# Performance work log

Measured on AMD Instinct MI355X. Metric: run time of the kernel, lower is better.

Reference implementation:

```python
import math
import jax, jax.numpy as jnp
from jax import lax
import numpy as np

SIZE = 5      # kernel size == num_gaussian
MUL = 16      # multiplicity of 0e and 1o in irreps_in/out
IN_DIM = 4 * MUL  # 16 scalars + 16 vectors = 64


def real_sh(v, xp=jnp):
    """Real spherical harmonics l=0..3, component normalization (||Y_l||^2=2l+1
    on unit vectors), homogeneous polynomial form so the zero vector maps to
    (1,0,...,0). v: (...,3) -> (...,16)."""
    x = v[..., 0]; y = v[..., 1]; z = v[..., 2]
    r2 = x * x + y * y + z * z
    s3 = math.sqrt(3.0); s5 = math.sqrt(5.0); s15 = math.sqrt(15.0)
    s7 = math.sqrt(7.0); s105 = math.sqrt(105.0)
    c21 = 0.5 * math.sqrt(10.5)   # (1/2)sqrt(21/2)
    c35 = 0.5 * math.sqrt(17.5)   # (1/2)sqrt(35/2)
    out = [
        xp.ones_like(x),
        s3 * y, s3 * z, s3 * x,
        s15 * x * y, s15 * y * z, 0.5 * s5 * (3 * z * z - r2),
        s15 * x * z, 0.5 * s15 * (x * x - y * y),
        c35 * y * (3 * x * x - y * y), s105 * x * y * z,
        c21 * y * (5 * z * z - r2), 0.5 * s7 * z * (5 * z * z - 3 * r2),
        c21 * x * (5 * z * z - r2), 0.5 * s105 * z * (x * x - y * y),
        c35 * x * (x * x - 3 * y * y),
    ]
    return xp.stack(out, axis=-1)


def _wigner3j(l1, l2, l3, rng):
    """Unit-Frobenius-norm SO(3)-invariant 3-tensor in the real SH basis above,
    found as the nullspace of rotation-invariance constraints (fp64 numpy)."""
    dims = (2 * l1 + 1, 2 * l2 + 1, 2 * l3 + 1)
    n = dims[0] * dims[1] * dims[2]
    rows = []
    for _ in range(4):
        A = rng.standard_normal((3, 3))
        Q, _ = np.linalg.qr(A)
        if np.linalg.det(Q) < 0:
            Q = -Q
        X = rng.standard_normal((64, 3))
        X /= np.linalg.norm(X, axis=1, keepdims=True)
        YA = real_sh(X, np)
        YB = real_sh(X @ Q.T, np)
        Ds = []
        for l in (l1, l2, l3):
            sl = slice(l * l, (l + 1) * (l + 1))
            D = np.linalg.lstsq(YA[:, sl], YB[:, sl], rcond=None)[0].T
            Ds.append(D)
        rows.append(np.kron(Ds[0], np.kron(Ds[1], Ds[2])) - np.eye(n))
    _, _, Vt = np.linalg.svd(np.concatenate(rows, 0))
    w = Vt[-1]
    w = w * np.sign(w[np.argmax(np.abs(w))])  # deterministic sign
    w = w / np.linalg.norm(w)
    return w.reshape(dims).astype(np.float32)

_rng = np.random.default_rng(7)
W3J = {k: jnp.asarray(_wigner3j(*k, _rng))
       for k in [(0, 0, 0), (0, 1, 1), (1, 0, 1), (1, 1, 0), (1, 2, 1)]}


def setup_inputs() -> dict:
    key = jax.random.key(0)
    k1, k2, k3, k4 = jax.random.split(key, 4)
    return {
        "x": jax.random.normal(k1, (4, IN_DIM, 32, 32, 32), jnp.float32),
        "w_lin0": jax.random.normal(k2, (MUL, MUL), jnp.float32),
        "w_lin1": jax.random.normal(k3, (MUL, MUL), jnp.float32),
        "tp_weight": jax.random.normal(k4, (SIZE, 5 * MUL * MUL), jnp.float32),
    }


def reference(x, w_lin0, w_lin1, tp_weight):
    size, mul = SIZE, MUL
    # --- lattice buffers (d, sh) ---
    r = jnp.linspace(-1.0, 1.0, size)
    lat = jnp.stack(jnp.meshgrid(r, r, r, indexing="ij"), axis=-1)  # (s,s,s,3)
    d = jnp.sqrt(jnp.sum(lat * lat, axis=-1))
    v = lat / jnp.maximum(d, 1e-12)[..., None]
    sh = real_sh(v)  # (s,s,s,16)
    # --- gaussian radial basis -> per-voxel tp weights ---
    centers = jnp.linspace(0.0, 1.0, size)
    sigma = 1.0 / (size - 1)
    emb = jnp.exp(-jnp.square((d[..., None] - centers) / sigma)) / 1.12
    w = (emb @ tp_weight) * jnp.cos(jnp.pi * d)[..., None] / size ** 1.5
    W = w.reshape(size, size, size, 5, mul, mul)  # 5 tp instructions
    # path normalization: sqrt((2l_out+1)/fan_in), fan_in = sum mul1*mul2 per output
    f0 = math.sqrt(1.0 / (2 * mul))   # 0e output: 2 paths of fan 16
    f1 = math.sqrt(3.0 / (3 * mul))   # 1o output: 3 paths of fan 16

    def blk(C, ysl, Wp, f):
        # C: (2l1+1,2l2+1,2l3+1); ysl: (s,s,s,2l2+1); Wp: (s,s,s,mul,mul)
        t = f * jnp.einsum("abc,xyzb,xyzuw->xyzuawc", C, ysl, Wp)
        s = t.shape
        return t.reshape(size, size, size, s[3] * s[4], s[5] * s[6])

    y0 = sh[..., 0:1]; y1 = sh[..., 1:4]; y2 = sh[..., 4:9]
    b00 = blk(W3J[(0, 0, 0)], y0, W[..., 0, :, :], f0)   # 0e->0e (16,16)
    b01 = blk(W3J[(0, 1, 1)], y1, W[..., 1, :, :], f1)   # 0e->1o (16,48)
    b11a = blk(W3J[(1, 0, 1)], y0, W[..., 2, :, :], f1)  # 1o->1o (48,48)
    b10 = blk(W3J[(1, 1, 0)], y1, W[..., 3, :, :], f0)   # 1o->0e (48,16)
    b11b = blk(W3J[(1, 2, 1)], y2, W[..., 4, :, :], f1)  # 1o->1o (48,48)
    k = jnp.concatenate([
        jnp.concatenate([b00, b01], axis=-1),
        jnp.concatenate([b10, b11a + b11b], axis=-1)], axis=-2)  # (s,s,s,64,64)
    kernel = jnp.transpose(k, (4, 3, 0, 1, 2))  # oixyz
    # --- self-interaction (e3nn Linear, per-l block, 1/sqrt(fan_in)) ---
    B = x.shape[0]
    sp = x.shape[2:]
    inv = 1.0 / math.sqrt(mul)
    x0 = x[:, :mul]
    x1 = x[:, mul:].reshape(B, mul, 3, *sp)
    si0 = inv * jnp.einsum("uv,buxyz->bvxyz", w_lin0, x0)
    si1 = inv * jnp.einsum("uv,bumxyz->bvmxyz", w_lin1, x1)
    si = jnp.concatenate([si0, si1.reshape(B, 3 * mul, *sp)], axis=1)
    # --- conv3d (cross-correlation, padding size//2) ---
    conv = lax.conv_general_dilated(
        x, kernel, window_strides=(1, 1, 1),
        padding=[(size // 2, size // 2)] * 3,
        dimension_numbers=("NCDHW", "OIDHW", "NCDHW"))
    return si + 0.1 * conv
```

## Files before the change

kernel.cpp:

```cpp
#include <hip/hip_runtime.h>
#include <math.h>

typedef __attribute__((ext_vector_type(8))) short bf16x8;
typedef __attribute__((ext_vector_type(16))) float f32x16;
typedef __attribute__((ext_vector_type(4))) unsigned int u32x4;

#define XB 131072

__device__ __forceinline__ unsigned f2bf(float f) {
    union { float f; unsigned u; } v; v.f = f;
    return (v.u + 0x7FFFu + ((v.u >> 16) & 1u)) >> 16;
}

template<int VM6, int LG>
__device__ __forceinline__ void waitcnt_fence() {
    __builtin_amdgcn_s_waitcnt((VM6 & 15) | ((VM6 >> 4) << 14) | (7 << 4) | (LG << 8));
    __builtin_amdgcn_sched_barrier(0);
}

__global__ __launch_bounds__(256) void prep(
    const float* __restrict__ w_lin0,
    const float* __restrict__ w_lin1,
    const float* __restrict__ tp_weight,
    unsigned short* __restrict__ Kb3,
    const float* __restrict__ x,
    unsigned short* __restrict__ xbz)
{
    __shared__ float wsh[1280];
    __shared__ float y1s[3];
    __shared__ float Qs[9];
    __shared__ __align__(16) char xpose[32768];

    const int tid = (int)threadIdx.x;
    const int blk = (int)blockIdx.x;

    if (blk < 128) {
        const int tap = blk;
#define KIDX(o, i) ((((i) >> 3) * 128 + tap) * 512 + (o) * 8 + ((i) & 7))
        if (tap >= 125) {
            for (int n = tid; n < 4096; n += 256)
                Kb3[(n >> 9) * 65536 + tap * 512 + (n & 511)] = 0;
            return;
        }
        const int i1 = tap / 25, i2 = (tap / 5) % 5, i3 = tap % 5;
        const float X = -1.0f + 0.5f * (float)i1;
        const float Y = -1.0f + 0.5f * (float)i2;
        const float Z = -1.0f + 0.5f * (float)i3;
        const float d = sqrtf(X*X + Y*Y + Z*Z);
        const float dinv = 1.0f / fmaxf(d, 1e-12f);
        const float vx = X * dinv, vy = Y * dinv, vz = Z * dinv;
        const float r2 = vx*vx + vy*vy + vz*vz;

        if (tid == 0) {
            const float s3 = 1.7320508075688772f;
            const float s15 = 3.872983346207417f;
            y1s[0] = s3 * vy; y1s[1] = s3 * vz; y1s[2] = s3 * vx;
            float y2v0 = s15 * vx * vy;
            float y2v1 = s15 * vy * vz;
            float y2v2 = 1.118033988749895f * (3.0f * vz * vz - r2);
            float y2v3 = s15 * vx * vz;
            float y2v4 = 1.9364916731037085f * (vx * vx - vy * vy);
            const float INV10 = 0.31622776601683794f;
            const float INV30 = 0.18257418583505536f;
            Qs[0] = -y2v2 * INV30 - y2v4 * INV10;
            Qs[4] =  2.0f * y2v2 * INV30;
            Qs[8] = -y2v2 * INV30 + y2v4 * INV10;
            Qs[1] = Qs[3] = y2v1 * INV10;
            Qs[2] = Qs[6] = y2v0 * INV10;
            Qs[5] = Qs[7] = y2v3 * INV10;
        }

        float emb[5];
        #pragma unroll
        for (int e = 0; e < 5; ++e) {
            float t = (d - 0.25f * (float)e) * 4.0f;
            emb[e] = expf(-t * t) * (1.0f / 1.12f);
        }
        const float scale = cosf(3.14159265358979323846f * d) / 11.180339887498949f;

        for (int j = tid; j < 1280; j += 256) {
            float s = 0.0f;
            #pragma unroll
            for (int e = 0; e < 5; ++e) s += emb[e] * tp_weight[e * 1280 + j];
            wsh[j] = scale * s;
        }
        __syncthreads();

        const float F0   = 0.17677669529663687f;
        const float F1   = 0.25f;
        const float F0S3 = 0.10206207261596574f;
        const float F1S3 = 0.14433756729740646f;

        #pragma unroll 1
        for (int n = 0; n < 16; ++n) {
            int e = n * 256 + tid;
            int o = e & 63, i = e >> 6;
            float Kv;
            if (o < 16) {
                if (i < 16) {
                    Kv = F0 * wsh[0 * 256 + i * 16 + o];
                } else {
                    int u = (i - 16) / 3, a = (i - 16) % 3;
                    Kv = F0S3 * y1s[a] * wsh[3 * 256 + u * 16 + o];
                }
            } else {
                int wcol = (o - 16) / 3, c = (o - 16) % 3;
                if (i < 16) {
                    Kv = F1S3 * y1s[c] * wsh[1 * 256 + i * 16 + wcol];
                } else {
                    int u = (i - 16) / 3, a = (i - 16) % 3;
                    Kv = F1 * Qs[a * 3 + c] * wsh[4 * 256 + u * 16 + wcol];
                    if (a == c) Kv += F1S3 * wsh[2 * 256 + u * 16 + wcol];
                }
            }
            if (tap == 62) {
                if (o < 16) {
                    if (i < 16) Kv += 2.5f * w_lin0[i * 16 + o];
                } else if (i >= 16) {
                    int v = (o - 16) / 3, m = (o - 16) % 3;
                    int u = (i - 16) / 3, a = (i - 16) % 3;
                    if (a == m) Kv += 2.5f * w_lin1[u * 16 + v];
                }
            }
            Kb3[KIDX(o, i)] = (unsigned short)f2bf(Kv);
        }
#undef KIDX
        return;
    }

    const int blk2 = blk - 128;
    if (blk2 == 0 && tid < 64) xbz[tid] = 0;
    const int p = blk2 * 256 + tid;
    const int b = p >> 15, pos = p & 32767;
    const float* xp = x + ((size_t)b << 21) + pos;

    u32x4 dv[8];
    #pragma unroll
    for (int cg = 0; cg < 8; ++cg) {
        #pragma unroll
        for (int jj = 0; jj < 4; ++jj) {
            float f0 = xp[((size_t)(cg * 8 + 2 * jj)) << 15];
            float f1 = xp[((size_t)(cg * 8 + 2 * jj + 1)) << 15];
            dv[cg][jj] = f2bf(f0) | (f2bf(f1) << 16);
        }
    }
    #pragma unroll
    for (int cg = 0; cg < 8; ++cg)
        *(u32x4*)&xpose[tid * 128 + ((cg ^ (tid & 7)) << 4)] = dv[cg];
    __syncthreads();

    const int w = tid >> 6, l = tid & 63, q = l >> 3, cg = l & 7;
    #pragma unroll
    for (int it = 0; it < 8; ++it) {
        int tsrc = w * 64 + it * 8 + q;
        u32x4 c = *(const u32x4*)&xpose[tsrc * 128 + ((cg ^ (tsrc & 7)) << 4)];
        *(u32x4*)((char*)xbz + 128 + ((size_t)(blk2 * 256 + tsrc)) * 128 + cg * 16) = c;
    }
}

template<int P, int PLAST>
__device__ __forceinline__ void kstep2(
    const int (&nbase)[2], int abase, bool thv,
    bf16x8 (&Ar)[2][2], bf16x8 (&Br)[2][2], f32x16 (&acc)[2][2])
{
    if constexpr (P < PLAST) {
        constexpr int Q = P + 1;
        constexpr int t0 = 2 * Q;
        constexpr int t1 = (2 * Q + 1 == 125) ? 124 : 2 * Q + 1;
        constexpr int dA = ((t0 / 25) * 160 + ((t0 / 5) % 5) * 20 + (t0 % 5)) * 16;
        constexpr int dB = ((t1 / 25) * 160 + ((t1 / 5) % 5) * 20 + (t1 % 5)) * 16;
        #pragma unroll
        for (int mo = 0; mo < 2; ++mo) {
            int a = Q * 2048 + abase + mo * 512;
            asm volatile("ds_read_b128 %0, %1" : "=v"(Ar[Q & 1][mo]) : "v"(a));
        }
        int dsel = thv ? dB : dA;
        #pragma unroll
        for (int np = 0; np < 2; ++np) {
            int a = nbase[np] + dsel;
            asm volatile("ds_read_b128 %0, %1" : "=v"(Br[Q & 1][np]) : "v"(a));
        }
    }
    waitcnt_fence<63, (P < PLAST) ? 4 : 0>();
    #pragma unroll
    for (int mo = 0; mo < 2; ++mo)
        #pragma unroll
        for (int np = 0; np < 2; ++np)
            acc[mo][np] = __builtin_amdgcn_mfma_f32_32x32x16_bf16(
                Ar[P & 1][mo], Br[P & 1][np], acc[mo][np], 0, 0, 0);
    if constexpr (P < PLAST)
        kstep2<P + 1, PLAST>(nbase, abase, thv, Ar, Br, acc);
}

template<int P0, int PLAST>
__device__ __forceinline__ void runphase(
    const int (&nbase)[2], int abase, bool thv, f32x16 (&acc)[2][2])
{
    bf16x8 Ar[2][2], Br[2][2];
    constexpr int t0 = 2 * P0, t1 = 2 * P0 + 1;
    constexpr int dA = ((t0 / 25) * 160 + ((t0 / 5) % 5) * 20 + (t0 % 5)) * 16;
    constexpr int dB = ((t1 / 25) * 160 + ((t1 / 5) % 5) * 20 + (t1 % 5)) * 16;
    #pragma unroll
    for (int mo = 0; mo < 2; ++mo) {
        int a = P0 * 2048 + abase + mo * 512;
        asm volatile("ds_read_b128 %0, %1" : "=v"(Ar[P0 & 1][mo]) : "v"(a));
    }
    int dsel = thv ? dB : dA;
    #pragma unroll
    for (int np = 0; np < 2; ++np) {
        int a = nbase[np] + dsel;
        asm volatile("ds_read_b128 %0, %1" : "=v"(Br[P0 & 1][np]) : "v"(a));
    }
    kstep2<P0, PLAST>(nbase, abase, thv, Ar, Br, acc);
}

__global__ __launch_bounds__(512, 1) void conv_mfma(
    const unsigned short* __restrict__ xbz,
    const unsigned short* __restrict__ Kb3,
    float* __restrict__ out)
{
    __shared__ __align__(16) char lds[161792];

    const int tid = (int)threadIdx.x;
    const int blk = (int)blockIdx.x;
    const int xt = blk & 1, yt = (blk >> 1) & 7, zt = (blk >> 4) & 3, b = blk >> 6;
    const int lane = tid & 63, wv = tid >> 6;
    const int l31 = lane & 31;
    const bool thv = (lane >= 32);

    unsigned srcOff[4];
    int xdst[4];
    {
        const int gz0 = zt * 8 - 2, gy0 = yt * 4 - 2, gx0 = xt * 16 - 2;
        #pragma unroll
        for (int i = 0; i < 4; ++i) {
            int c = tid + i * 512;
            if (c >= 1920) c -= 1920;
            int hz = c / 160; int rem = c - hz * 160;
            int hy = rem / 20;  int hx = rem - hy * 20;
            int gz = gz0 + hz, gy = gy0 + hy, gx = gx0 + hx;
            bool ok = ((unsigned)gz < 32u) && ((unsigned)gy < 32u) && ((unsigned)gx < 32u);
            int pg = (gz << 10) + (gy << 5) + gx;
            srcOff[i] = ok ? (unsigned)(128 + (((b << 15) + pg) << 7)) : 0u;
            xdst[i] = XB + c * 16;
        }
    }

    const int abase = l31 * 16 + (thv ? 1024 : 0);
    int nbase[2];
    #pragma unroll
    for (int np = 0; np < 2; ++np)
        nbase[np] = XB + (wv * 160 + ((l31 >> 4) + 2 * np) * 20 + (l31 & 15)) * 16;

    f32x16 acc[2][2];
    #pragma unroll
    for (int i = 0; i < 2; ++i)
        #pragma unroll
        for (int j = 0; j < 2; ++j) acc[i][j] = (f32x16)0.0f;

    const char* kb = (const char*)Kb3;
    const int kchunk = tid * 16;

    #pragma unroll
    for (int j = 0; j < 8; ++j) {
        __builtin_amdgcn_global_load_lds(
            (const __attribute__((address_space(1))) unsigned int*)(kb + kchunk + j * 8192),
            (__attribute__((address_space(3))) unsigned int*)(lds + kchunk + j * 8192),
            16, 0, 0);
    }
    #pragma unroll
    for (int i = 0; i < 4; ++i) {
        __builtin_amdgcn_global_load_lds(
            (const __attribute__((address_space(1))) unsigned int*)
                ((const char*)xbz + srcOff[i]),
            (__attribute__((address_space(3))) unsigned int*)(lds + xdst[i]),
            16, 0, 0);
    }

    u32x4 xr[4];

    #pragma unroll 1
    for (int s = 0; s < 8; ++s) {
        const char* kbs = kb + s * 131072;

        __builtin_amdgcn_s_barrier();
        __builtin_amdgcn_sched_barrier(0);
        if (s > 0) {
            waitcnt_fence<8, 15>();
            #pragma unroll
            for (int i = 0; i < 4; ++i)
                asm volatile("ds_write_b128 %0, %1" :: "v"(xdst[i]), "v"(xr[i]));
        }
        #pragma unroll
        for (int j = 0; j < 8; ++j) {
            __builtin_amdgcn_global_load_lds(
                (const __attribute__((address_space(1))) unsigned int*)
                    (kbs + 65536 + kchunk + j * 8192),
                (__attribute__((address_space(3))) unsigned int*)
                    (lds + 65536 + kchunk + j * 8192),
                16, 0, 0);
        }
        waitcnt_fence<8, 0>();
        __builtin_amdgcn_s_barrier();
        __builtin_amdgcn_sched_barrier(0);

        {
            unsigned sx = (unsigned)(((s < 7) ? s + 1 : 7) * 16);
            #pragma unroll
            for (int i = 0; i < 4; ++i) {
                unsigned voff = srcOff[i] + sx;
                asm volatile("global_load_dwordx4 %0, %1, %2"
                             : "=v"(xr[i]) : "v"(voff), "s"(xbz));
            }
            __builtin_amdgcn_sched_barrier(0);
        }

        runphase<0, 31>(nbase, abase, thv, acc);

        __builtin_amdgcn_s_barrier();
        __builtin_amdgcn_sched_barrier(0);
        #pragma unroll
        for (int j = 0; j < 8; ++j) {
            __builtin_amdgcn_global_load_lds(
                (const __attribute__((address_space(1))) unsigned int*)
                    (kbs + 131072 + kchunk + j * 8192),
                (__attribute__((address_space(3))) unsigned int*)
                    (lds + kchunk + j * 8192),
                16, 0, 0);
        }
        waitcnt_fence<12, 15>();
        __builtin_amdgcn_s_barrier();
        __builtin_amdgcn_sched_barrier(0);

        runphase<32, 62>(nbase, abase, thv, acc);
    }

    const int gz = zt * 8 + wv;
    #pragma unroll
    for (int mo = 0; mo < 2; ++mo) {
        #pragma unroll
        for (int np = 0; np < 2; ++np) {
            const int gy = yt * 4 + 2 * np + (l31 >> 4);
            const int gx = xt * 16 + (l31 & 15);
            #pragma unroll
            for (int reg = 0; reg < 16; ++reg) {
                int o = mo * 32 + (reg & 3) + 8 * (reg >> 2) + (thv ? 4 : 0);
                out[(((size_t)(b * 64 + o)) << 15) + (gz << 10) + (gy << 5) + gx] =
                    0.1f * acc[mo][np][reg];
            }
        }
    }
}

extern "C" void kernel_launch(void* const* d_in, const int* in_sizes, int n_in,
                              void* d_out, int out_size, void* d_ws, size_t ws_size,
                              hipStream_t stream) {
    const float* x       = (const float*)d_in[0];
    const float* w_lin0  = (const float*)d_in[1];
    const float* w_lin1  = (const float*)d_in[2];
    const float* tp      = (const float*)d_in[3];
    unsigned short* Kb3 = (unsigned short*)d_ws;
    unsigned short* xbz = (unsigned short*)((char*)d_ws + (2u << 20));
    float* out = (float*)d_out;

    prep<<<640, 256, 0, stream>>>(w_lin0, w_lin1, tp, Kb3, x, xbz);
    conv_mfma<<<256, 512, 0, stream>>>(xbz, Kb3, out);
}
```

Measured before the change: 128.9 us.

## Fuse prep and conv into one cooperative kernel with grid sync

Merges the weight/input preparation kernel and the MFMA convolution kernel into a single cooperative launch. Each 512-thread block runs two prep sub-blocks, one per 256-thread half, then issues a grid-wide barrier before the convolution phase. This removes the second kernel launch and the gap between kernels. In exchange it adds a grid sync, depends on all 256 blocks being co-resident, and the prep work now runs at lower parallelism (256 blocks instead of 640).

```diff
diff --git a/kernel.cpp b/kernel.cpp
--- a/kernel.cpp
+++ b/kernel.cpp
@@ -1,5 +1,8 @@
 #include <hip/hip_runtime.h>
+#include <hip/hip_cooperative_groups.h>
 #include <math.h>
+
+namespace cg = cooperative_groups;
 
 typedef __attribute__((ext_vector_type(8))) short bf16x8;
 typedef __attribute__((ext_vector_type(16))) float f32x16;
@@ -16,146 +19,6 @@
 __device__ __forceinline__ void waitcnt_fence() {
     __builtin_amdgcn_s_waitcnt((VM6 & 15) | ((VM6 >> 4) << 14) | (7 << 4) | (LG << 8));
     __builtin_amdgcn_sched_barrier(0);
-}
-
-__global__ __launch_bounds__(256) void prep(
-    const float* __restrict__ w_lin0,
-    const float* __restrict__ w_lin1,
-    const float* __restrict__ tp_weight,
-    unsigned short* __restrict__ Kb3,
-    const float* __restrict__ x,
-    unsigned short* __restrict__ xbz)
-{
-    __shared__ float wsh[1280];
-    __shared__ float y1s[3];
-    __shared__ float Qs[9];
-    __shared__ __align__(16) char xpose[32768];
-
-    const int tid = (int)threadIdx.x;
-    const int blk = (int)blockIdx.x;
-
-    if (blk < 128) {
-        const int tap = blk;
-#define KIDX(o, i) ((((i) >> 3) * 128 + tap) * 512 + (o) * 8 + ((i) & 7))
-        if (tap >= 125) {
-            for (int n = tid; n < 4096; n += 256)
-                Kb3[(n >> 9) * 65536 + tap * 512 + (n & 511)] = 0;
-            return;
-        }
-        const int i1 = tap / 25, i2 = (tap / 5) % 5, i3 = tap % 5;
-        const float X = -1.0f + 0.5f * (float)i1;
-        const float Y = -1.0f + 0.5f * (float)i2;
-        const float Z = -1.0f + 0.5f * (float)i3;
-        const float d = sqrtf(X*X + Y*Y + Z*Z);
-        const float dinv = 1.0f / fmaxf(d, 1e-12f);
-        const float vx = X * dinv, vy = Y * dinv, vz = Z * dinv;
-        const float r2 = vx*vx + vy*vy + vz*vz;
-
-        if (tid == 0) {
-            const float s3 = 1.7320508075688772f;
-            const float s15 = 3.872983346207417f;
-            y1s[0] = s3 * vy; y1s[1] = s3 * vz; y1s[2] = s3 * vx;
-            float y2v0 = s15 * vx * vy;
-            float y2v1 = s15 * vy * vz;
-            float y2v2 = 1.118033988749895f * (3.0f * vz * vz - r2);
-            float y2v3 = s15 * vx * vz;
-            float y2v4 = 1.9364916731037085f * (vx * vx - vy * vy);
-            const float INV10 = 0.31622776601683794f;
-            const float INV30 = 0.18257418583505536f;
-            Qs[0] = -y2v2 * INV30 - y2v4 * INV10;
-            Qs[4] =  2.0f * y2v2 * INV30;
-            Qs[8] = -y2v2 * INV30 + y2v4 * INV10;
-            Qs[1] = Qs[3] = y2v1 * INV10;
-            Qs[2] = Qs[6] = y2v0 * INV10;
-            Qs[5] = Qs[7] = y2v3 * INV10;
-        }
-
-        float emb[5];
-        #pragma unroll
-        for (int e = 0; e < 5; ++e) {
-            float t = (d - 0.25f * (float)e) * 4.0f;
-            emb[e] = expf(-t * t) * (1.0f / 1.12f);
-        }
-        const float scale = cosf(3.14159265358979323846f * d) / 11.180339887498949f;
-
-        for (int j = tid; j < 1280; j += 256) {
-            float s = 0.0f;
-            #pragma unroll
-            for (int e = 0; e < 5; ++e) s += emb[e] * tp_weight[e * 1280 + j];
-            wsh[j] = scale * s;
-        }
-        __syncthreads();
-
-        const float F0   = 0.17677669529663687f;
-        const float F1   = 0.25f;
-        const float F0S3 = 0.10206207261596574f;
-        const float F1S3 = 0.14433756729740646f;
-
-        #pragma unroll 1
-        for (int n = 0; n < 16; ++n) {
-            int e = n * 256 + tid;
-            int o = e & 63, i = e >> 6;
-            float Kv;
-            if (o < 16) {
-                if (i < 16) {
-                    Kv = F0 * wsh[0 * 256 + i * 16 + o];
-                } else {
-                    int u = (i - 16) / 3, a = (i - 16) % 3;
-                    Kv = F0S3 * y1s[a] * wsh[3 * 256 + u * 16 + o];
-                }
-            } else {
-                int wcol = (o - 16) / 3, c = (o - 16) % 3;
-                if (i < 16) {
-                    Kv = F1S3 * y1s[c] * wsh[1 * 256 + i * 16 + wcol];
-                } else {
-                    int u = (i - 16) / 3, a = (i - 16) % 3;
-                    Kv = F1 * Qs[a * 3 + c] * wsh[4 * 256 + u * 16 + wcol];
-                    if (a == c) Kv += F1S3 * wsh[2 * 256 + u * 16 + wcol];
-                }
-            }
-            if (tap == 62) {
-                if (o < 16) {
-                    if (i < 16) Kv += 2.5f * w_lin0[i * 16 + o];
-                } else if (i >= 16) {
-                    int v = (o - 16) / 3, m = (o - 16) % 3;
-                    int u = (i - 16) / 3, a = (i - 16) % 3;
-                    if (a == m) Kv += 2.5f * w_lin1[u * 16 + v];
-                }
-            }
-            Kb3[KIDX(o, i)] = (unsigned short)f2bf(Kv);
-        }
-#undef KIDX
-        return;
-    }
-
-    const int blk2 = blk - 128;
-    if (blk2 == 0 && tid < 64) xbz[tid] = 0;
-    const int p = blk2 * 256 + tid;
-    const int b = p >> 15, pos = p & 32767;
-    const float* xp = x + ((size_t)b << 21) + pos;
-
-    u32x4 dv[8];
-    #pragma unroll
-    for (int cg = 0; cg < 8; ++cg) {
-        #pragma unroll
-        for (int jj = 0; jj < 4; ++jj) {
-            float f0 = xp[((size_t)(cg * 8 + 2 * jj)) << 15];
-            float f1 = xp[((size_t)(cg * 8 + 2 * jj + 1)) << 15];
-            dv[cg][jj] = f2bf(f0) | (f2bf(f1) << 16);
-        }
-    }
-    #pragma unroll
-    for (int cg = 0; cg < 8; ++cg)
-        *(u32x4*)&xpose[tid * 128 + ((cg ^ (tid & 7)) << 4)] = dv[cg];
-    __syncthreads();
-
-    const int w = tid >> 6, l = tid & 63, q = l >> 3, cg = l & 7;
-    #pragma unroll
-    for (int it = 0; it < 8; ++it) {
-        int tsrc = w * 64 + it * 8 + q;
-        u32x4 c = *(const u32x4*)&xpose[tsrc * 128 + ((cg ^ (tsrc & 7)) << 4)];
-        *(u32x4*)((char*)xbz + 128 + ((size_t)(blk2 * 256 + tsrc)) * 128 + cg * 16) = c;
-    }
 }
 
 template<int P, int PLAST>
@@ -214,15 +77,157 @@
     kstep2<P0, PLAST>(nbase, abase, thv, Ar, Br, acc);
 }
 
-__global__ __launch_bounds__(512, 1) void conv_mfma(
-    const unsigned short* __restrict__ xbz,
-    const unsigned short* __restrict__ Kb3,
+__global__ __launch_bounds__(512, 1) void fused(
+    const float* __restrict__ w_lin0,
+    const float* __restrict__ w_lin1,
+    const float* __restrict__ tp_weight,
+    unsigned short* __restrict__ Kb3,
+    const float* __restrict__ x,
+    unsigned short* __restrict__ xbz,
     float* __restrict__ out)
 {
     __shared__ __align__(16) char lds[161792];
 
     const int tid = (int)threadIdx.x;
     const int blk = (int)blockIdx.x;
+
+    {
+        const int sub = tid >> 8;
+        const int stid = tid & 255;
+        char* xpose = lds + sub * 32768;
+        float* wshp = (float*)(lds + 65536 + sub * 8192);
+        float* y1p  = (float*)(lds + 81920 + sub * 128);
+        float* Qp   = y1p + 4;
+
+        const int xblk = blk * 2 + sub;
+        if (xblk == 0 && stid < 64) xbz[stid] = 0;
+        const int p = xblk * 256 + stid;
+        const int xb = p >> 15, pos = p & 32767;
+        const float* xp = x + ((size_t)xb << 21) + pos;
+        u32x4 dv[8];
+        #pragma unroll
+        for (int cgi = 0; cgi < 8; ++cgi) {
+            #pragma unroll
+            for (int jj = 0; jj < 4; ++jj) {
+                float f0 = xp[((size_t)(cgi * 8 + 2 * jj)) << 15];
+                float f1 = xp[((size_t)(cgi * 8 + 2 * jj + 1)) << 15];
+                dv[cgi][jj] = f2bf(f0) | (f2bf(f1) << 16);
+            }
+        }
+        #pragma unroll
+        for (int cgi = 0; cgi < 8; ++cgi)
+            *(u32x4*)&xpose[stid * 128 + ((cgi ^ (stid & 7)) << 4)] = dv[cgi];
+
+        const int tap = blk * 2 + sub;
+        const bool doKb = (blk < 64);
+        const bool kzero = (tap >= 125);
+        if (doKb && !kzero) {
+            const int i1 = tap / 25, i2 = (tap / 5) % 5, i3 = tap % 5;
+            const float X = -1.0f + 0.5f * (float)i1;
+            const float Y = -1.0f + 0.5f * (float)i2;
+            const float Z = -1.0f + 0.5f * (float)i3;
+            const float d = sqrtf(X*X + Y*Y + Z*Z);
+            const float dinv = 1.0f / fmaxf(d, 1e-12f);
+            const float vx = X * dinv, vy = Y * dinv, vz = Z * dinv;
+            const float r2 = vx*vx + vy*vy + vz*vz;
+            if (stid == 0) {
+                const float s3 = 1.7320508075688772f;
+                const float s15 = 3.872983346207417f;
+                y1p[0] = s3 * vy; y1p[1] = s3 * vz; y1p[2] = s3 * vx;
+                float y2v0 = s15 * vx * vy;
+                float y2v1 = s15 * vy * vz;
+                float y2v2 = 1.118033988749895f * (3.0f * vz * vz - r2);
+                float y2v3 = s15 * vx * vz;
+                float y2v4 = 1.9364916731037085f * (vx * vx - vy * vy);
+                const float INV10 = 0.31622776601683794f;
+                const float INV30 = 0.18257418583505536f;
+                Qp[0] = -y2v2 * INV30 - y2v4 * INV10;
+                Qp[4] =  2.0f * y2v2 * INV30;
+                Qp[8] = -y2v2 * INV30 + y2v4 * INV10;
+                Qp[1] = Qp[3] = y2v1 * INV10;
+                Qp[2] = Qp[6] = y2v0 * INV10;
+                Qp[5] = Qp[7] = y2v3 * INV10;
+            }
+            float emb[5];
+            #pragma unroll
+            for (int e = 0; e < 5; ++e) {
+                float t = (d - 0.25f * (float)e) * 4.0f;
+                emb[e] = expf(-t * t) * (1.0f / 1.12f);
+            }
+            const float scale = cosf(3.14159265358979323846f * d) / 11.180339887498949f;
+            for (int j = stid; j < 1280; j += 256) {
+                float s = 0.0f;
+                #pragma unroll
+                for (int e = 0; e < 5; ++e) s += emb[e] * tp_weight[e * 1280 + j];
+                wshp[j] = scale * s;
+            }
+        }
+        __syncthreads();
+
+        {
+            const int w = tid >> 6, l = tid & 63, q = l >> 3, cgi = l & 7;
+            char* xpw = lds + (w >> 2) * 32768;
+            const int xblkw = blk * 2 + (w >> 2);
+            #pragma unroll
+            for (int it = 0; it < 8; ++it) {
+                int tsrc = (w & 3) * 64 + it * 8 + q;
+                u32x4 c = *(const u32x4*)&xpw[tsrc * 128 + ((cgi ^ (tsrc & 7)) << 4)];
+                *(u32x4*)((char*)xbz + 128 +
+                          ((size_t)(xblkw * 256 + tsrc)) * 128 + cgi * 16) = c;
+            }
+        }
+
+        if (doKb) {
+#define KIDX(o, i) ((((i) >> 3) * 128 + tap) * 512 + (o) * 8 + ((i) & 7))
+            if (kzero) {
+                for (int n = stid; n < 4096; n += 256)
+                    Kb3[(n >> 9) * 65536 + tap * 512 + (n & 511)] = 0;
+            } else {
+                const float F0   = 0.17677669529663687f;
+                const float F1   = 0.25f;
+                const float F0S3 = 0.10206207261596574f;
+                const float F1S3 = 0.14433756729740646f;
+                #pragma unroll 1
+                for (int n = 0; n < 16; ++n) {
+                    int e = n * 256 + stid;
+                    int o = e & 63, i = e >> 6;
+                    float Kv;
+                    if (o < 16) {
+                        if (i < 16) {
+                            Kv = F0 * wshp[0 * 256 + i * 16 + o];
+                        } else {
+                            int u = (i - 16) / 3, a = (i - 16) % 3;
+                            Kv = F0S3 * y1p[a] * wshp[3 * 256 + u * 16 + o];
+                        }
+                    } else {
+                        int wcol = (o - 16) / 3, c = (o - 16) % 3;
+                        if (i < 16) {
+                            Kv = F1S3 * y1p[c] * wshp[1 * 256 + i * 16 + wcol];
+                        } else {
+                            int u = (i - 16) / 3, a = (i - 16) % 3;
+                            Kv = F1 * Qp[a * 3 + c] * wshp[4 * 256 + u * 16 + wcol];
+                            if (a == c) Kv += F1S3 * wshp[2 * 256 + u * 16 + wcol];
+                        }
+                    }
+                    if (tap == 62) {
+                        if (o < 16) {
+                            if (i < 16) Kv += 2.5f * w_lin0[i * 16 + o];
+                        } else if (i >= 16) {
+                            int v = (o - 16) / 3, m = (o - 16) % 3;
+                            int u = (i - 16) / 3, a = (i - 16) % 3;
+                            if (a == m) Kv += 2.5f * w_lin1[u * 16 + v];
+                        }
+                    }
+                    Kb3[KIDX(o, i)] = (unsigned short)f2bf(Kv);
+                }
+            }
+#undef KIDX
+        }
+    }
+
+    __threadfence();
+    cg::this_grid().sync();
+
     const int xt = blk & 1, yt = (blk >> 1) & 7, zt = (blk >> 4) & 3, b = blk >> 6;
     const int lane = tid & 63, wv = tid >> 6;
     const int l31 = lane & 31;
@@ -363,6 +368,8 @@
     unsigned short* xbz = (unsigned short*)((char*)d_ws + (2u << 20));
     float* out = (float*)d_out;
 
-    prep<<<640, 256, 0, stream>>>(w_lin0, w_lin1, tp, Kb3, x, xbz);
-    conv_mfma<<<256, 512, 0, stream>>>(xbz, Kb3, out);
-}
+    void* args[] = { (void*)&w_lin0, (void*)&w_lin1, (void*)&tp,
+                     (void*)&Kb3, (void*)&x, (void*)&xbz, (void*)&out };
+    hipLaunchCooperativeKernel((const void*)fused, dim3(256), dim3(512),
+                               args, 0, stream);
+}
```

Result: slower. 234.9 us (+82.2%).
